# Optimization experiments

Measured on AMD Instinct MI355X. Metric: run time of the kernel, lower is better.

## Reference

```python
import jax, jax.numpy as jnp
import numpy as np

B, T, D = 4, 1024, 1024
H = 16                      # attention heads
DS, DC, EXP = 16, 4, 2      # d_state, d_conv, expand
DIN = EXP * D               # 2048
DTR = D // 16               # dt_rank = 64
TOPK_RATIO = 0.25
EPS = 1e-5


def setup_inputs() -> dict:
    key = jax.random.key(0)
    ks = jax.random.split(key, 16)
    def n(k, shape, scale=0.02):
        return jax.random.normal(k, shape, jnp.float32) * scale
    return {
        "x": jax.random.normal(ks[0], (B, T, D), jnp.float32),
        "ln_w": jnp.ones((D,), jnp.float32),
        "ln_b": jnp.zeros((D,), jnp.float32),
        "r_w1": n(ks[1], (D, D // 2)),
        "r_b1": jnp.zeros((D // 2,), jnp.float32),
        "r_w2": n(ks[2], (D // 2, 1)),
        "r_b2": jnp.zeros((1,), jnp.float32),
        "Wq": n(ks[3], (D, D)), "bq": jnp.zeros((D,), jnp.float32),
        "Wk": n(ks[4], (D, D)), "bk": jnp.zeros((D,), jnp.float32),
        "Wv": n(ks[5], (D, D)), "bv": jnp.zeros((D,), jnp.float32),
        "Wo": n(ks[6], (D, D)), "bo": jnp.zeros((D,), jnp.float32),
        "in_w": n(ks[7], (D, 2 * DIN)),
        "conv_w": n(ks[8], (DIN, DC), 0.1),
        "conv_b": jnp.zeros((DIN,), jnp.float32),
        "xproj_w": n(ks[9], (DIN, DTR + 2 * DS)),
        "dt_w": n(ks[10], (DTR, DIN), 0.1),
        "dt_b": jnp.full((DIN,), -4.0, jnp.float32) + n(ks[11], (DIN,), 0.1),
        "A_log": jnp.log(jnp.broadcast_to(jnp.arange(1, DS + 1, dtype=jnp.float32), (DIN, DS))),
        "Dp": jnp.ones((DIN,), jnp.float32),
        "out_w": n(ks[12], (DIN, D)),
    }


def _attn_core(x, Wq, bq, Wk, bk, Wv, bv, Wo, bo):
    b, L, d = x.shape
    hd = d // H
    q = (x @ Wq + bq).reshape(b, L, H, hd)
    k = (x @ Wk + bk).reshape(b, L, H, hd)
    v = (x @ Wv + bv).reshape(b, L, H, hd)
    scores = jnp.einsum('bqhd,bkhd->bhqk', q, k) / jnp.sqrt(jnp.float32(hd))
    p = jax.nn.softmax(scores, axis=-1)
    o = jnp.einsum('bhqk,bkhd->bqhd', p, v).reshape(b, L, d)
    return o @ Wo + bo


def _ssm_core(u, in_w, conv_w, conv_b, xproj_w, dt_w, dt_b, A_log, Dp, out_w):
    # Mamba-style selective SSM on the sub-sequence u: (b, L, D)
    b, L, _ = u.shape
    xi, z = jnp.split(u @ in_w, 2, axis=-1)            # (b, L, DIN) each
    xp = jnp.pad(xi, ((0, 0), (DC - 1, 0), (0, 0)))    # causal depthwise conv1d
    xc = conv_b + sum(xp[:, j:j + L] * conv_w[:, j] for j in range(DC))
    xc = jax.nn.silu(xc)
    proj = xc @ xproj_w                                # (b, L, DTR + 2*DS)
    dtp = proj[..., :DTR]
    Bm = proj[..., DTR:DTR + DS]
    Cm = proj[..., DTR + DS:]
    delta = jax.nn.softplus(dtp @ dt_w + dt_b)         # (b, L, DIN)
    A = -jnp.exp(A_log)                                # (DIN, DS)
    dA = jnp.exp(delta[..., None] * A)                 # (b, L, DIN, DS)
    dBu = (delta * xc)[..., None] * Bm[:, :, None, :]  # (b, L, DIN, DS)

    def step(h, inp):
        dA_t, dBu_t, C_t = inp
        h = dA_t * h + dBu_t                           # (b, DIN, DS)
        return h, jnp.einsum('bds,bs->bd', h, C_t)

    xs = (jnp.moveaxis(dA, 1, 0), jnp.moveaxis(dBu, 1, 0), jnp.moveaxis(Cm, 1, 0))
    _, ys = jax.lax.scan(step, jnp.zeros((b, DIN, DS), u.dtype), xs)
    y = jnp.moveaxis(ys, 0, 1) + xc * Dp               # (b, L, DIN)
    y = y * jax.nn.silu(z)
    return y @ out_w


def reference(x, ln_w, ln_b, r_w1, r_b1, r_w2, r_b2, Wq, bq, Wk, bk, Wv, bv, Wo, bo,
              in_w, conv_w, conv_b, xproj_w, dt_w, dt_b, A_log, Dp, out_w):
    b, t, d = x.shape
    k = min(max(1, int(TOPK_RATIO * t)), t)            # static top-k count
    # pre-norm (LayerNorm)
    mu = x.mean(-1, keepdims=True)
    var = ((x - mu) ** 2).mean(-1, keepdims=True)
    xn = (x - mu) * jax.lax.rsqrt(var + EPS) * ln_w + ln_b
    # router scores (b, t) and top-k dispatch
    scores = jnp.squeeze(jax.nn.gelu(xn @ r_w1 + r_b1) @ r_w2 + r_b2, -1)
    _, topk_idx = jax.lax.top_k(scores, k)
    bidx = jnp.arange(b)[:, None]
    mask = jnp.zeros((b, t), bool).at[bidx, topk_idx].set(True)
    # unselected positions in ascending order (stable sort of 0/1 mask)
    order = jnp.argsort(mask.astype(jnp.int32), axis=1)
    bottom_idx = order[:, :t - k]
    # SSM branch on bottom (t-k) tokens, order-preserving
    x_ssm = xn[bidx, bottom_idx]                       # (b, t-k, d)
    d_ssm_tok = _ssm_core(x_ssm, in_w, conv_w, conv_b, xproj_w, dt_w, dt_b, A_log, Dp, out_w)
    delta_ssm = jnp.zeros_like(xn).at[bidx, bottom_idx].set(d_ssm_tok)
    # attention branch on top-k tokens only (sparse attention)
    x_attn = xn[bidx, topk_idx]                        # (b, k, d)
    d_attn_tok = _attn_core(x_attn, Wq, bq, Wk, bk, Wv, bv, Wo, bo)
    delta_attn = jnp.zeros_like(xn).at[bidx, topk_idx].set(d_attn_tok)
    # masked merge + residual
    delta = jnp.where(mask[..., None], delta_attn, delta_ssm)
    return x + delta
```

## Files before the change

### kernel.cpp

```cpp
#include <hip/hip_runtime.h>
#include <hip/hip_bf16.h>
#include <cstdint>
#include <cstddef>

typedef unsigned short u16;
typedef __attribute__((ext_vector_type(8))) short short8;
typedef __attribute__((ext_vector_type(4))) float f32x4;

__device__ __forceinline__ float b2f(u16 h){ union{unsigned u; float f;} c; c.u = ((unsigned)h)<<16; return c.f; }
__device__ __forceinline__ u16 f2b(float f){ union{float f; unsigned u;} c; c.f = f; unsigned u = c.u; return (u16)((u + 0x7fffu + ((u>>16)&1u)) >> 16); }
__device__ __forceinline__ float gelu_f(float x){
  float x3 = x*x*x;
  return 0.5f*x*(1.f + tanhf(0.7978845608028654f*(x + 0.044715f*x3)));
}
__device__ __forceinline__ void gload_lds16(const void* g, void* l){
  __builtin_amdgcn_global_load_lds((const __attribute__((address_space(1))) void*)g,
                                   (__attribute__((address_space(3))) void*)l, 16, 0, 0);
}

__global__ __launch_bounds__(256) void k_ln(const float* __restrict__ x, const float* __restrict__ w,
    const float* __restrict__ b, float* __restrict__ xn, u16* __restrict__ apk)
{
  int t = blockIdx.x, tid = threadIdx.x;
  float4 v = ((const float4*)(x + (size_t)t*1024))[tid];
  float s = v.x+v.y+v.z+v.w;
  #pragma unroll
  for (int o=32;o;o>>=1) s += __shfl_xor(s,o,64);
  __shared__ float r1[4], r2[4];
  if ((tid&63)==0) r1[tid>>6] = s;
  __syncthreads();
  float mu = (r1[0]+r1[1]+r1[2]+r1[3]) * (1.f/1024.f);
  float4 c = {v.x-mu, v.y-mu, v.z-mu, v.w-mu};
  float q = c.x*c.x+c.y*c.y+c.z*c.z+c.w*c.w;
  #pragma unroll
  for (int o=32;o;o>>=1) q += __shfl_xor(q,o,64);
  if ((tid&63)==0) r2[tid>>6] = q;
  __syncthreads();
  float inv = rsqrtf((r2[0]+r2[1]+r2[2]+r2[3])*(1.f/1024.f) + 1e-5f);
  float4 wv = ((const float4*)w)[tid];
  float4 bv = ((const float4*)b)[tid];
  float4 o4 = {c.x*inv*wv.x+bv.x, c.y*inv*wv.y+bv.y, c.z*inv*wv.z+bv.z, c.w*inv*wv.w+bv.w};
  ((float4*)(xn + (size_t)t*1024))[tid] = o4;
  union{u16 u[4]; uint2 d;} hi, lo;
  float xs[4] = {o4.x, o4.y, o4.z, o4.w};
  #pragma unroll
  for (int e=0;e<4;e++){ u16 h = f2b(xs[e]); hi.u[e]=h; lo.u[e]=f2b(xs[e]-b2f(h)); }
  u16* row = apk + (size_t)t*3072;
  int k4 = tid*4;
  *(uint2*)&row[k4]      = hi.d;
  *(uint2*)&row[1024+k4] = hi.d;
  *(uint2*)&row[2048+k4] = lo.d;
}

__global__ __launch_bounds__(256) void k_tcvt(const float* __restrict__ src, u16* __restrict__ dst, int R, int C)
{
  __shared__ float tile[32][33];
  int c0 = blockIdx.x*32, r0 = blockIdx.y*32;
  int lc = threadIdx.x & 31, lr = threadIdx.x >> 5;
  #pragma unroll
  for (int rr=0; rr<4; rr++) tile[lr + rr*8][lc] = src[(size_t)(r0 + lr + rr*8)*C + c0 + lc];
  __syncthreads();
  #pragma unroll
  for (int rr=0; rr<4; rr++) dst[(size_t)(c0 + lr + rr*8)*R + r0 + lc] = f2b(tile[lc][lr + rr*8]);
}

__global__ __launch_bounds__(256) void k_bpack(const float* __restrict__ bq, const float* __restrict__ bk,
    const float* __restrict__ bv, float* __restrict__ o)
{
  int i = blockIdx.x*256 + threadIdx.x;
  o[i] = (i < 1024) ? bq[i] : ((i < 2048) ? bk[i-1024] : bv[i-2048]);
}

__global__ __launch_bounds__(256) void k_splitB(const float* __restrict__ w1, u16* __restrict__ bp)
{
  __shared__ float tile[32][33];
  int n0 = blockIdx.x*32, k0 = blockIdx.y*32;
  int lc = threadIdx.x & 31, lr = threadIdx.x >> 5;
  #pragma unroll
  for (int rr=0; rr<4; rr++) tile[lr+rr*8][lc] = w1[(size_t)(k0+lr+rr*8)*512 + n0+lc];
  __syncthreads();
  #pragma unroll
  for (int rr=0; rr<4; rr++){
    int n = n0 + lr + rr*8, k = k0 + lc;
    float x = tile[lc][lr+rr*8];
    u16 hi = f2b(x);
    u16 lo = f2b(x - b2f(hi));
    u16* row = bp + (size_t)n*3072;
    row[k] = hi; row[1024+k] = lo; row[2048+k] = hi;
  }
}

__global__ __launch_bounds__(256) void k_score3(const float* __restrict__ ps, const float* __restrict__ b2,
    float* __restrict__ scores)
{
  int i = blockIdx.x*256 + threadIdx.x;
  float s = b2[0];
  #pragma unroll
  for (int p=0;p<16;p++) s += ps[p*4096 + i];
  scores[i] = s;
}

__global__ __launch_bounds__(1024) void k_topk(const float* __restrict__ scores, int* __restrict__ aidx, int* __restrict__ sidx)
{
  int b = blockIdx.x, tid = threadIdx.x;
  __shared__ float s[1024];
  __shared__ int pf[1024];
  s[tid] = scores[b*1024 + tid];
  __syncthreads();
  float my = s[tid];
  int cnt = 0;
  for (int j=0;j<1024;j++){ float sj = s[j]; cnt += (sj > my) || (sj == my && j < tid); }
  int isa = (cnt < 256) ? 1 : 0;
  pf[tid] = isa; __syncthreads();
  for (int o=1;o<1024;o<<=1){
    int add = (tid >= o) ? pf[tid-o] : 0;
    __syncthreads();
    pf[tid] += add;
    __syncthreads();
  }
  int excl = pf[tid] - isa;
  if (isa) aidx[b*256 + excl] = tid;
  else     sidx[b*768 + (tid - excl)] = tid;
}

__global__ __launch_bounds__(256) void k_gather(const float* __restrict__ xn, const int* __restrict__ aidx,
    const int* __restrict__ sidx, u16* __restrict__ xat, u16* __restrict__ xst)
{
  int id = blockIdx.x;
  int b = id >> 10, s = id & 1023;
  int src; u16* dst;
  if (s < 256) { src = aidx[b*256 + s]; dst = xat + (size_t)(b*256 + s)*1024; }
  else { int ss = s - 256; src = sidx[b*768 + ss]; dst = xst + (size_t)(b*768 + ss)*1024; }
  const float4* sp = (const float4*)(xn + ((size_t)b*1024 + src)*1024);
  int tid = threadIdx.x;
  float4 vv = sp[tid];
  union { u16 u[4]; uint2 d; } pk;
  pk.u[0]=f2b(vv.x); pk.u[1]=f2b(vv.y); pk.u[2]=f2b(vv.z); pk.u[3]=f2b(vv.w);
  ((uint2*)dst)[tid] = pk.d;
}

template<int BM, int BN>
__global__ __launch_bounds__(256) void k_mfma(const u16* __restrict__ A, int lda,
    const u16* __restrict__ Bt, int ldb, const float* __restrict__ bias,
    float* __restrict__ outf, u16* __restrict__ outb, int M, int N, int K,
    int act, int split)
{
  constexpr int WTM = BM/2, WTN = BN/2;
  constexpr int MI = WTM/16, NJ = WTN/16;
  __shared__ u16 lA[2][BM*32];
  __shared__ u16 lB[2][BN*32];
  const int tid = threadIdx.x;
  const int lane = tid & 63;
  const int wv = tid >> 6;
  const int wm = wv >> 1, wn = wv & 1;
  const int r0 = lane & 15;
  const int kg = lane >> 4;

  int bx = blockIdx.x, by = blockIdx.y;
  if (gridDim.z == 1) {
    int nwg = gridDim.x * gridDim.y;
    int f = by * gridDim.x + bx;
    int q = nwg >> 3, r = nwg & 7;
    int xcd = f & 7, ord = f >> 3;
    int base = (xcd < r) ? xcd*(q+1) : r*(q+1) + (xcd - r)*q;
    int lin = base + ord;
    bx = lin % gridDim.x;
    by = lin / gridDim.x;
  }
  const int tm = bx * BM, tn = by * BN;

  const int ksl = K / gridDim.z;
  const int kbeg = blockIdx.z * ksl;
  if (gridDim.z > 1) outf += (size_t)blockIdx.z * ((size_t)M * N);

  auto stage = [&](int buf, int kt){
    for (int c = tid; c < BM*4; c += 256) {
      int row = c >> 2, j = c & 3;
      int jj = j ^ ((row >> 1) & 3);
      gload_lds16(&A[(size_t)(tm + row)*lda + kt + jj*8], &lA[buf][c*8]);
    }
    for (int c = tid; c < BN*4; c += 256) {
      int row = c >> 2, j = c & 3;
      int jj = j ^ ((row >> 1) & 3);
      gload_lds16(&Bt[(size_t)(tn + row)*ldb + kt + jj*8], &lB[buf][c*8]);
    }
  };

  f32x4 acc[MI][NJ];
  #pragma unroll
  for (int i=0;i<MI;i++)
    #pragma unroll
    for (int j=0;j<NJ;j++) acc[i][j] = (f32x4){0.f,0.f,0.f,0.f};

  stage(0, kbeg);
  __syncthreads();
  const int nk = ksl / 32;
  int cur = 0;
  for (int t = 0; t < nk; t++) {
    if (t + 1 < nk) stage(cur ^ 1, kbeg + (t+1)*32);
    short8 av[MI], bvv[NJ];
    #pragma unroll
    for (int i=0;i<MI;i++){
      int row = wm*WTM + i*16 + r0;
      av[i] = *(const short8*)&lA[cur][row*32 + ((kg ^ ((row>>1)&3))<<3)];
    }
    #pragma unroll
    for (int j=0;j<NJ;j++){
      int row = wn*WTN + j*16 + r0;
      bvv[j] = *(const short8*)&lB[cur][row*32 + ((kg ^ ((row>>1)&3))<<3)];
    }
    #pragma unroll
    for (int i=0;i<MI;i++)
      #pragma unroll
      for (int j=0;j<NJ;j++)
        acc[i][j] = __builtin_amdgcn_mfma_f32_16x16x32_bf16(av[i], bvv[j], acc[i][j], 0, 0, 0);
    __syncthreads();
    cur ^= 1;
  }

  if (act == 3) {
    const float* w2 = (const float*)outb;
    #pragma unroll
    for (int i=0;i<MI;i++){
      #pragma unroll
      for (int r=0;r<4;r++){
        float t = 0.f;
        #pragma unroll
        for (int j=0;j<NJ;j++){
          int col = tn + wn*WTN + j*16 + r0;
          t += gelu_f(acc[i][j][r] + bias[col]) * w2[col];
        }
        #pragma unroll
        for (int o=1;o<16;o<<=1) t += __shfl_xor(t, o, 64);
        if (r0 == 0)
          outf[(size_t)(by*2 + wn)*M + tm + wm*WTM + i*16 + kg*4 + r] = t;
      }
    }
    return;
  }

  const int rr = kg * 4;
  #pragma unroll
  for (int i=0;i<MI;i++){
    #pragma unroll
    for (int j=0;j<NJ;j++){
      #pragma unroll
      for (int r=0;r<4;r++){
        int row = tm + wm*WTM + i*16 + rr + r;
        int col = tn + wn*WTN + j*16 + r0;
        float v = acc[i][j][r];
        if (bias) v += bias[col];
        if (act == 1) v = (v > 15.f) ? v : log1pf(__expf(v));
        else if (act == 2) v = gelu_f(v);
        if (col < split) outf[(size_t)row*split + col] = v;
        else             outb[(size_t)row*(N-split) + (col-split)] = f2b(v);
      }
    }
  }
}

__global__ __launch_bounds__(256) void k_psum(const float* __restrict__ p, float* __restrict__ o,
    u16* __restrict__ dtpb)
{
  int i = blockIdx.x*256 + threadIdx.x;
  float v = p[i] + p[i+294912] + p[i+589824] + p[i+884736];
  o[i] = v;
  int tok = i / 96, col = i - tok*96;
  if (col < 64) dtpb[tok*64 + col] = f2b(v);
}

__global__ __launch_bounds__(256) void k_attn2(const u16* __restrict__ qkv, u16* __restrict__ ob)
{
  __shared__ u16 lKP[16384];
  __shared__ u16 lVt[16384];
  char* KP = (char*)lKP;
  char* VT = (char*)lVt;
  const int tid = threadIdx.x;
  const int lane = tid & 63;
  const int w = tid >> 6;
  const int bx = blockIdx.x;
  const int b = bx >> 6, h = (bx >> 2) & 15, ch = bx & 3;

  const u16* kbase = qkv + (size_t)(b*256)*3072 + 1024 + h*64;
  const u16* vbase = qkv + (size_t)(b*256)*3072 + 2048 + h*64;

  {
    int rr = tid >> 3;
    int c8 = (tid & 7) * 8;
    for (int i = 0; i < 8; i++) {
      int row = i*32 + rr;
      int4 kv = *(const int4*)&kbase[(size_t)row*3072 + c8];
      int koff = row*128 + c8*2;
      *(int4*)(KP + (koff ^ ((row & 7) << 4))) = kv;
      int4 vv = *(const int4*)&vbase[(size_t)row*3072 + c8];
      union { int4 q; u16 u[8]; } vu; vu.q = vv;
      #pragma unroll
      for (int jj = 0; jj < 8; jj++) {
        int j = (jj + rr) & 7;
        int d = c8 + j;
        int voff = d*512 + row*2;
        *(u16*)(VT + (voff ^ ((d & 7) << 4))) = vu.u[j];
      }
    }
  }

  const int r0 = lane & 15;
  const int kg = lane >> 4;
  const int qrow = ch*64 + w*16 + r0;
  const u16* qp = qkv + (size_t)(b*256 + qrow)*3072 + h*64 + kg*8;
  short8 qf0 = *(const short8*)(qp);
  short8 qf1 = *(const short8*)(qp + 32);

  __syncthreads();

  f32x4 acc[16];
  #pragma unroll
  for (int t = 0; t < 16; t++) acc[t] = (f32x4){0.f,0.f,0.f,0.f};
  #pragma unroll
  for (int t = 0; t < 16; t++) {
    int row = t*16 + r0;
    int base = row*128 + kg*16;
    short8 kf0 = *(const short8*)(KP + ((base     ) ^ ((row & 7) << 4)));
    short8 kf1 = *(const short8*)(KP + ((base + 64) ^ ((row & 7) << 4)));
    acc[t] = __builtin_amdgcn_mfma_f32_16x16x32_bf16(qf0, kf0, acc[t], 0, 0, 0);
    acc[t] = __builtin_amdgcn_mfma_f32_16x16x32_bf16(qf1, kf1, acc[t], 0, 0, 0);
  }

  #pragma unroll
  for (int t = 0; t < 16; t++) acc[t] = acc[t] * 0.125f;
  float lsum[4];
  #pragma unroll
  for (int r = 0; r < 4; r++) {
    float mx = -1e30f;
    #pragma unroll
    for (int t = 0; t < 16; t++) mx = fmaxf(mx, acc[t][r]);
    #pragma unroll
    for (int o = 1; o < 16; o <<= 1) mx = fmaxf(mx, __shfl_xor(mx, o, 64));
    float s = 0.f;
    #pragma unroll
    for (int t = 0; t < 16; t++) { float p = __expf(acc[t][r] - mx); acc[t][r] = p; s += p; }
    #pragma unroll
    for (int o = 1; o < 16; o <<= 1) s += __shfl_xor(s, o, 64);
    lsum[r] = s;
  }

  __syncthreads();
  char* PW = KP + w*8192;
  #pragma unroll
  for (int t = 0; t < 16; t++) {
    int col = t*16 + r0;
    #pragma unroll
    for (int r = 0; r < 4; r++) {
      int row = kg*4 + r;
      int off = row*512 + col*2;
      *(u16*)(PW + (off ^ ((row & 7) << 4))) = f2b(acc[t][r]);
    }
  }

  f32x4 oacc[4];
  #pragma unroll
  for (int dt = 0; dt < 4; dt++) oacc[dt] = (f32x4){0.f,0.f,0.f,0.f};
  #pragma unroll
  for (int kc = 0; kc < 8; kc++) {
    int pbase = r0*512 + kc*64 + kg*16;
    short8 pf = *(const short8*)(PW + (pbase ^ ((r0 & 7) << 4)));
    #pragma unroll
    for (int dt = 0; dt < 4; dt++) {
      int vrow = dt*16 + r0;
      int vb2 = vrow*512 + kc*64 + kg*16;
      short8 vf = *(const short8*)(VT + (vb2 ^ ((vrow & 7) << 4)));
      oacc[dt] = __builtin_amdgcn_mfma_f32_16x16x32_bf16(pf, vf, oacc[dt], 0, 0, 0);
    }
  }

  u16* op = ob + (size_t)(b*256 + ch*64 + w*16)*1024 + h*64;
  #pragma unroll
  for (int dt = 0; dt < 4; dt++) {
    #pragma unroll
    for (int r = 0; r < 4; r++) {
      int row = kg*4 + r;
      float v = oacc[dt][r] / lsum[r];
      op[(size_t)row*1024 + dt*16 + r0] = f2b(v);
    }
  }
}

__global__ __launch_bounds__(256) void k_conv(const float* __restrict__ xi, const float* __restrict__ cw,
    const float* __restrict__ cb, u16* __restrict__ xcb)
{
  size_t idx = (size_t)blockIdx.x*256 + threadIdx.x;
  int d = (int)(idx & 2047);
  size_t bt = idx >> 11;
  int t = (int)(bt % 768);
  float acc = cb[d];
  const float* p = xi + idx;
  float w0=cw[d*4+0], w1=cw[d*4+1], w2=cw[d*4+2], w3=cw[d*4+3];
  acc += w3 * p[0];
  if (t >= 1) acc += w2 * p[-2048];
  if (t >= 2) acc += w1 * p[-4096];
  if (t >= 3) acc += w0 * p[-6144];
  float sv = acc / (1.f + __expf(-acc));
  xcb[idx] = f2b(sv);
}

__global__ __launch_bounds__(256) void k_scan1(const u16* __restrict__ delta, const u16* __restrict__ xcb,
    const float* __restrict__ proj, const float* __restrict__ A_log, float* __restrict__ cs)
{
  int bid = blockIdx.x;
  int db = bid & 7;
  int c  = (bid >> 3) & 15;
  int b  = bid >> 7;
  int d  = db*256 + threadIdx.x;
  float Ar[16];
  #pragma unroll
  for (int s=0;s<16;s++) Ar[s] = -__expf(A_log[d*16+s]);
  float ap[16], hc[16];
  #pragma unroll
  for (int s=0;s<16;s++){ ap[s]=1.f; hc[s]=0.f; }
  size_t row0 = (size_t)b*768 + c*48;
  for (int t=0;t<48;t++){
    size_t row = row0 + t;
    float dl = b2f(delta[row*2048 + d]);
    float xv = b2f(xcb[row*2048 + d]);
    float du = dl*xv;
    const float4* bp = (const float4*)&proj[row*96 + 64];
    float4 b0 = bp[0], b1 = bp[1], b2 = bp[2], b3 = bp[3];
    float Bc[16] = {b0.x,b0.y,b0.z,b0.w,b1.x,b1.y,b1.z,b1.w,
                    b2.x,b2.y,b2.z,b2.w,b3.x,b3.y,b3.z,b3.w};
    #pragma unroll
    for (int s=0;s<16;s++){
      float dA = __expf(dl*Ar[s]);
      ap[s] *= dA;
      hc[s] = dA*hc[s] + du*Bc[s];
    }
  }
  size_t base = ((size_t)(b*16 + c)*32)*2048 + d;
  #pragma unroll
  for (int s=0;s<16;s++){
    cs[base + (size_t)s*2048]      = ap[s];
    cs[base + (size_t)(16+s)*2048] = hc[s];
  }
}

__global__ __launch_bounds__(256) void k_scan2(float* __restrict__ cs)
{
  int bid = blockIdx.x;
  int db = bid & 7;
  int s  = (bid >> 3) & 15;
  int b  = bid >> 7;
  int d  = db*256 + threadIdx.x;
  float h = 0.f;
  for (int c=0;c<16;c++){
    size_t base = ((size_t)(b*16 + c)*32)*2048 + d;
    float ap = cs[base + (size_t)s*2048];
    float hc = cs[base + (size_t)(16+s)*2048];
    cs[base + (size_t)(16+s)*2048] = h;
    h = ap*h + hc;
  }
}

__global__ __launch_bounds__(256) void k_scan3(const u16* __restrict__ delta, const u16* __restrict__ xcb,
    const float* __restrict__ proj, const float* __restrict__ cs, const u16* __restrict__ zb,
    const float* __restrict__ A_log, const float* __restrict__ Dp, u16* __restrict__ yb)
{
  int bid = blockIdx.x;
  int db = bid & 7;
  int c  = (bid >> 3) & 15;
  int b  = bid >> 7;
  int d  = db*256 + threadIdx.x;
  float Ar[16];
  #pragma unroll
  for (int s=0;s<16;s++) Ar[s] = -__expf(A_log[d*16+s]);
  float dpv = Dp[d];
  float h[16];
  size_t base = ((size_t)(b*16 + c)*32)*2048 + d;
  #pragma unroll
  for (int s=0;s<16;s++) h[s] = cs[base + (size_t)(16+s)*2048];
  size_t row0 = (size_t)b*768 + c*48;
  for (int t=0;t<48;t++){
    size_t row = row0 + t;
    float dl = b2f(delta[row*2048 + d]);
    float xv = b2f(xcb[row*2048 + d]);
    float du = dl*xv;
    const float4* bp = (const float4*)&proj[row*96 + 64];
    float4 b0 = bp[0], b1 = bp[1], b2 = bp[2], b3 = bp[3];
    const float4* cp = (const float4*)&proj[row*96 + 80];
    float4 c0 = cp[0], c1 = cp[1], c2 = cp[2], c3 = cp[3];
    float Bc[16] = {b0.x,b0.y,b0.z,b0.w,b1.x,b1.y,b1.z,b1.w,
                    b2.x,b2.y,b2.z,b2.w,b3.x,b3.y,b3.z,b3.w};
    float Cc[16] = {c0.x,c0.y,c0.z,c0.w,c1.x,c1.y,c1.z,c1.w,
                    c2.x,c2.y,c2.z,c2.w,c3.x,c3.y,c3.z,c3.w};
    float y = 0.f;
    #pragma unroll
    for (int s=0;s<16;s++){
      float dA = __expf(dl*Ar[s]);
      h[s] = dA*h[s] + du*Bc[s];
      y += h[s]*Cc[s];
    }
    y += xv*dpv;
    float z = b2f(zb[row*2048 + d]);
    float g = z / (1.f + __expf(-z));
    yb[row*2048 + d] = f2b(y*g);
  }
}

__global__ __launch_bounds__(256) void k_scat(const float* __restrict__ x, const int* __restrict__ idxarr,
    const float* __restrict__ dlt, float* __restrict__ out, int per_b)
{
  int id = blockIdx.x;
  int b = id / per_b;
  int t = idxarr[id];
  const float4* xp = (const float4*)(x + ((size_t)b*1024 + t)*1024);
  const float4* dp = (const float4*)(dlt + (size_t)id*1024);
  float4* op = (float4*)(out + ((size_t)b*1024 + t)*1024);
  int tid = threadIdx.x;
  float4 a = xp[tid], d = dp[tid];
  op[tid] = (float4){a.x+d.x, a.y+d.y, a.z+d.z, a.w+d.w};
}

extern "C" void kernel_launch(void* const* d_in, const int* in_sizes, int n_in,
                              void* d_out, int out_size, void* d_ws, size_t ws_size,
                              hipStream_t stream)
{
  const float* x      = (const float*)d_in[0];
  const float* ln_w   = (const float*)d_in[1];
  const float* ln_b   = (const float*)d_in[2];
  const float* r_w1   = (const float*)d_in[3];
  const float* r_b1   = (const float*)d_in[4];
  const float* r_w2   = (const float*)d_in[5];
  const float* r_b2   = (const float*)d_in[6];
  const float* Wq     = (const float*)d_in[7];
  const float* bq     = (const float*)d_in[8];
  const float* Wk     = (const float*)d_in[9];
  const float* bk     = (const float*)d_in[10];
  const float* Wv     = (const float*)d_in[11];
  const float* bv     = (const float*)d_in[12];
  const float* Wo     = (const float*)d_in[13];
  const float* bo     = (const float*)d_in[14];
  const float* in_w   = (const float*)d_in[15];
  const float* conv_w = (const float*)d_in[16];
  const float* conv_b = (const float*)d_in[17];
  const float* xproj_w= (const float*)d_in[18];
  const float* dt_w   = (const float*)d_in[19];
  const float* dt_b   = (const float*)d_in[20];
  const float* A_log  = (const float*)d_in[21];
  const float* Dp     = (const float*)d_in[22];
  const float* out_w  = (const float*)d_in[23];
  float* out = (float*)d_out;

  uint8_t* ws = (uint8_t*)d_ws;
  size_t off = 0;
  auto alloc = [&](size_t bytes)->uint8_t*{
    uint8_t* p = ws + off;
    off += (bytes + 255) & ~(size_t)255;
    return p;
  };

  float* xn    = (float*)alloc(4096ull*1024*4);
  u16*   wqt   = (u16*)  alloc(1024ull*1024*2);
  u16*   wkt   = (u16*)  alloc(1024ull*1024*2);
  u16*   wvt   = (u16*)  alloc(1024ull*1024*2);
  u16*   wot   = (u16*)  alloc(1024ull*1024*2);
  u16*   inwt  = (u16*)  alloc(4096ull*1024*2);
  u16*   outwt = (u16*)  alloc(1024ull*2048*2);
  u16*   xpwt  = (u16*)  alloc(96ull*2048*2);
  u16*   dtwt  = (u16*)  alloc(2048ull*64*2);
  u16*   r1pk  = (u16*)  alloc(512ull*3072*2);
  float* scores= (float*)alloc(4096*4);
  int*   aidx  = (int*)  alloc(1024*4);
  int*   sidx  = (int*)  alloc(3072*4);
  u16*   xat   = (u16*)  alloc(1024ull*1024*2);
  u16*   xst   = (u16*)  alloc(3072ull*1024*2);
  float* qkvb  = (float*)alloc(3072*4);

  float* s_projp = xn;
  float* cs = xn;

  uint8_t* arena = ws + off;
  u16*   apk = (u16*)(arena);
  float* ps  = (float*)(arena + 25165824);
  u16*   qkvbuf = (u16*)(arena);
  u16*   obuf   = (u16*)(arena + 6291456);
  float* adelta = (float*)(arena + 8388608);
  float* s_xi   = (float*)(arena);
  u16*   s_zb   = (u16*)(arena + 25165824);
  u16*   s_xcb  = (u16*)(arena + 62914560);
  float* s_proj = (float*)(arena + 75497472);
  u16*   s_dtpb = (u16*)(arena + 76677120);
  u16*   s_deltab = (u16*)s_xi;
  u16*   s_yb     = s_xcb;
  float* s_sdelta = (float*)s_zb;

  hipLaunchKernelGGL(k_ln, dim3(4096), dim3(256), 0, stream, x, ln_w, ln_b, xn, apk);
  hipLaunchKernelGGL(k_tcvt, dim3(32,32),  dim3(256), 0, stream, Wq,     wqt,   1024, 1024);
  hipLaunchKernelGGL(k_tcvt, dim3(32,32),  dim3(256), 0, stream, Wk,     wkt,   1024, 1024);
  hipLaunchKernelGGL(k_tcvt, dim3(32,32),  dim3(256), 0, stream, Wv,     wvt,   1024, 1024);
  hipLaunchKernelGGL(k_tcvt, dim3(32,32),  dim3(256), 0, stream, Wo,     wot,   1024, 1024);
  hipLaunchKernelGGL(k_tcvt, dim3(128,32), dim3(256), 0, stream, in_w,   inwt,  1024, 4096);
  hipLaunchKernelGGL(k_tcvt, dim3(32,64),  dim3(256), 0, stream, out_w,  outwt, 2048, 1024);
  hipLaunchKernelGGL(k_tcvt, dim3(3,64),   dim3(256), 0, stream, xproj_w,xpwt,  2048, 96);
  hipLaunchKernelGGL(k_tcvt, dim3(64,2),   dim3(256), 0, stream, dt_w,   dtwt,  64,   2048);
  hipLaunchKernelGGL(k_bpack, dim3(12), dim3(256), 0, stream, bq, bk, bv, qkvb);
  hipLaunchKernelGGL(k_splitB, dim3(16,32), dim3(256), 0, stream, r_w1, r1pk);
  hipLaunchKernelGGL((k_mfma<64,64>), dim3(64,8), dim3(256), 0, stream,
      apk, 3072, r1pk, 3072, r_b1, ps, (u16*)r_w2, 4096, 512, 3072, 3, 0);
  hipLaunchKernelGGL(k_score3, dim3(16), dim3(256), 0, stream, ps, r_b2, scores);
  hipLaunchKernelGGL(k_topk, dim3(4), dim3(1024), 0, stream, scores, aidx, sidx);
  hipLaunchKernelGGL(k_gather, dim3(4096), dim3(256), 0, stream, xn, aidx, sidx, xat, xst);
  hipLaunchKernelGGL((k_mfma<32,128>), dim3(32,24), dim3(256), 0, stream,
      xat, 1024, wqt, 1024, qkvb, (float*)nullptr, qkvbuf, 1024, 3072, 1024, 0, 0);
  hipLaunchKernelGGL(k_attn2, dim3(256), dim3(256), 0, stream, qkvbuf, obuf);
  hipLaunchKernelGGL((k_mfma<32,64>), dim3(32,16), dim3(256), 0, stream,
      obuf, 1024, wot, 1024, bo, adelta, (u16*)nullptr, 1024, 1024, 1024, 0, 1024);
  hipLaunchKernelGGL(k_scat, dim3(1024), dim3(256), 0, stream, x, aidx, adelta, out, 256);
  hipLaunchKernelGGL((k_mfma<128,128>), dim3(24,32), dim3(256), 0, stream,
      xst, 1024, inwt, 1024, (const float*)nullptr, s_xi, s_zb, 3072, 4096, 1024, 0, 2048);
  hipLaunchKernelGGL(k_conv, dim3(24576), dim3(256), 0, stream, s_xi, conv_w, conv_b, s_xcb);
  hipLaunchKernelGGL((k_mfma<32,96>), dim3(96,1,4), dim3(256), 0, stream,
      s_xcb, 2048, xpwt, 2048, (const float*)nullptr, s_projp, (u16*)nullptr, 3072, 96, 2048, 0, 96);
  hipLaunchKernelGGL(k_psum, dim3(1152), dim3(256), 0, stream, s_projp, s_proj, s_dtpb);
  hipLaunchKernelGGL((k_mfma<64,128>), dim3(48,16), dim3(256), 0, stream,
      s_dtpb, 64, dtwt, 64, dt_b, (float*)nullptr, s_deltab, 3072, 2048, 64, 1, 0);
  hipLaunchKernelGGL(k_scan1, dim3(512), dim3(256), 0, stream, s_deltab, s_xcb, s_proj, A_log, cs);
  hipLaunchKernelGGL(k_scan2, dim3(512), dim3(256), 0, stream, cs);
  hipLaunchKernelGGL(k_scan3, dim3(512), dim3(256), 0, stream, s_deltab, s_xcb, s_proj, cs, s_zb, A_log, Dp, s_yb);
  hipLaunchKernelGGL((k_mfma<32,128>), dim3(96,8), dim3(256), 0, stream,
      s_yb, 2048, outwt, 2048, (const float*)nullptr, s_sdelta, (u16*)nullptr, 3072, 1024, 2048, 0, 1024);
  hipLaunchKernelGGL(k_scat, dim3(3072), dim3(256), 0, stream, x, sidx, s_sdelta, out, 768);
}
```

Before: 448.4 us.

## Store SSM in-proj xi as bf16, vectorize conv, drop XCD remap

The in-projection GEMM now writes both the xi and z halves as bf16 into one contiguous buffer, instead of writing xi as fp32. The depthwise conv reads that bf16 data four channels per thread with vector loads and stores. The GEMM tile shrinks from 128x128 to 64x128, and the XCD-aware block swizzle is removed from every GEMM launch. The workspace layout is rearranged to fit the new buffers. These changes cut the memory traffic of the xi intermediate and the conv, but xi loses precision, and dropping the swizzle may hurt L2 locality on the multi-XCD chip.

```diff
diff --git a/kernel.cpp b/kernel.cpp
--- a/kernel.cpp
+++ b/kernel.cpp
@@ -153,21 +153,9 @@
   const int lane = tid & 63;
   const int wv = tid >> 6;
   const int wm = wv >> 1, wn = wv & 1;
+  const int tm = blockIdx.x * BM, tn = blockIdx.y * BN;
   const int r0 = lane & 15;
   const int kg = lane >> 4;
-
-  int bx = blockIdx.x, by = blockIdx.y;
-  if (gridDim.z == 1) {
-    int nwg = gridDim.x * gridDim.y;
-    int f = by * gridDim.x + bx;
-    int q = nwg >> 3, r = nwg & 7;
-    int xcd = f & 7, ord = f >> 3;
-    int base = (xcd < r) ? xcd*(q+1) : r*(q+1) + (xcd - r)*q;
-    int lin = base + ord;
-    bx = lin % gridDim.x;
-    by = lin / gridDim.x;
-  }
-  const int tm = bx * BM, tn = by * BN;
 
   const int ksl = K / gridDim.z;
   const int kbeg = blockIdx.z * ksl;
@@ -233,7 +221,7 @@
         #pragma unroll
         for (int o=1;o<16;o<<=1) t += __shfl_xor(t, o, 64);
         if (r0 == 0)
-          outf[(size_t)(by*2 + wn)*M + tm + wm*WTM + i*16 + kg*4 + r] = t;
+          outf[(size_t)(blockIdx.y*2 + wn)*M + tm + wm*WTM + i*16 + kg*4 + r] = t;
       }
     }
     return;
@@ -252,8 +240,12 @@
         if (bias) v += bias[col];
         if (act == 1) v = (v > 15.f) ? v : log1pf(__expf(v));
         else if (act == 2) v = gelu_f(v);
-        if (col < split) outf[(size_t)row*split + col] = v;
-        else             outb[(size_t)row*(N-split) + (col-split)] = f2b(v);
+        if (col < split) {
+          if (outf) outf[(size_t)row*split + col] = v;
+          else      outb[(size_t)row*split + col] = f2b(v);
+        } else {
+          outb[(outf ? (size_t)0 : (size_t)M*split) + (size_t)row*(N-split) + (col-split)] = f2b(v);
+        }
       }
     }
   }
@@ -385,22 +377,29 @@
   }
 }
 
-__global__ __launch_bounds__(256) void k_conv(const float* __restrict__ xi, const float* __restrict__ cw,
+__global__ __launch_bounds__(256) void k_conv(const u16* __restrict__ xib, const float* __restrict__ cw,
     const float* __restrict__ cb, u16* __restrict__ xcb)
 {
-  size_t idx = (size_t)blockIdx.x*256 + threadIdx.x;
-  int d = (int)(idx & 2047);
-  size_t bt = idx >> 11;
+  size_t e4 = ((size_t)blockIdx.x*256 + threadIdx.x) * 4;
+  int d = (int)(e4 & 2047);
+  size_t bt = e4 >> 11;
   int t = (int)(bt % 768);
-  float acc = cb[d];
-  const float* p = xi + idx;
-  float w0=cw[d*4+0], w1=cw[d*4+1], w2=cw[d*4+2], w3=cw[d*4+3];
-  acc += w3 * p[0];
-  if (t >= 1) acc += w2 * p[-2048];
-  if (t >= 2) acc += w1 * p[-4096];
-  if (t >= 3) acc += w0 * p[-6144];
-  float sv = acc / (1.f + __expf(-acc));
-  xcb[idx] = f2b(sv);
+  float acc[4];
+  #pragma unroll
+  for (int e=0;e<4;e++) acc[e] = cb[d+e];
+  #pragma unroll
+  for (int k=0;k<4;k++){
+    if (t >= k) {
+      union{uint2 v; u16 u[4];} ld;
+      ld.v = *(const uint2*)&xib[e4 - (size_t)k*2048];
+      #pragma unroll
+      for (int e=0;e<4;e++) acc[e] += cw[(d+e)*4 + (3-k)] * b2f(ld.u[e]);
+    }
+  }
+  union{u16 u[4]; uint2 v;} o;
+  #pragma unroll
+  for (int e=0;e<4;e++){ float sv = acc[e] / (1.f + __expf(-acc[e])); o.u[e] = f2b(sv); }
+  *(uint2*)&xcb[e4] = o.v;
 }
 
 __global__ __launch_bounds__(256) void k_scan1(const u16* __restrict__ delta, const u16* __restrict__ xcb,
@@ -582,14 +581,14 @@
   u16*   qkvbuf = (u16*)(arena);
   u16*   obuf   = (u16*)(arena + 6291456);
   float* adelta = (float*)(arena + 8388608);
-  float* s_xi   = (float*)(arena);
-  u16*   s_zb   = (u16*)(arena + 25165824);
+  u16*   s_xib  = (u16*)(arena);
+  u16*   s_zb   = s_xib + 3072ull*2048;
+  u16*   s_deltab = (u16*)(arena + 37748736);
   u16*   s_xcb  = (u16*)(arena + 62914560);
   float* s_proj = (float*)(arena + 75497472);
   u16*   s_dtpb = (u16*)(arena + 76677120);
-  u16*   s_deltab = (u16*)s_xi;
   u16*   s_yb     = s_xcb;
-  float* s_sdelta = (float*)s_zb;
+  float* s_sdelta = (float*)arena;
 
   hipLaunchKernelGGL(k_ln, dim3(4096), dim3(256), 0, stream, x, ln_w, ln_b, xn, apk);
   hipLaunchKernelGGL(k_tcvt, dim3(32,32),  dim3(256), 0, stream, Wq,     wqt,   1024, 1024);
@@ -613,9 +612,9 @@
   hipLaunchKernelGGL((k_mfma<32,64>), dim3(32,16), dim3(256), 0, stream,
       obuf, 1024, wot, 1024, bo, adelta, (u16*)nullptr, 1024, 1024, 1024, 0, 1024);
   hipLaunchKernelGGL(k_scat, dim3(1024), dim3(256), 0, stream, x, aidx, adelta, out, 256);
-  hipLaunchKernelGGL((k_mfma<128,128>), dim3(24,32), dim3(256), 0, stream,
-      xst, 1024, inwt, 1024, (const float*)nullptr, s_xi, s_zb, 3072, 4096, 1024, 0, 2048);
-  hipLaunchKernelGGL(k_conv, dim3(24576), dim3(256), 0, stream, s_xi, conv_w, conv_b, s_xcb);
+  hipLaunchKernelGGL((k_mfma<64,128>), dim3(48,32), dim3(256), 0, stream,
+      xst, 1024, inwt, 1024, (const float*)nullptr, (float*)nullptr, s_xib, 3072, 4096, 1024, 0, 2048);
+  hipLaunchKernelGGL(k_conv, dim3(6144), dim3(256), 0, stream, s_xib, conv_w, conv_b, s_xcb);
   hipLaunchKernelGGL((k_mfma<32,96>), dim3(96,1,4), dim3(256), 0, stream,
       s_xcb, 2048, xpwt, 2048, (const float*)nullptr, s_projp, (u16*)nullptr, 3072, 96, 2048, 0, 96);
   hipLaunchKernelGGL(k_psum, dim3(1152), dim3(256), 0, stream, s_projp, s_proj, s_dtpb);
```

After: 485.1 us. +8.2%, slower.
